# Kernel tuning notes

Hardware: AMD Instinct MI355X
Metric: run time of the kernel (lower is better)

The kernel has to match this reference:

```python
import jax, jax.numpy as jnp
import numpy as np

N, E, DN, DE, H, L = 2048, 32768, 512, 512, 8, 2
BN_EPS = 1e-5  # torch BatchNorm1d eps; eval mode with running_mean=0, running_var=1


def setup_inputs():
    key = jax.random.key(0)
    ks = jax.random.split(key, 12)
    rng = np.random.default_rng(0)
    # unique directed edges: 3E/4 upper-triangular pairs + reverses of the first E/4
    iu, ju = np.triu_indices(N, k=1)
    sel = rng.choice(iu.size, size=3 * E // 4, replace=False)
    s, d = iu[sel], ju[sel]
    src = np.concatenate([s, d[: E // 4]])
    dst = np.concatenate([d, s[: E // 4]])
    edge_index = jnp.asarray(np.stack([src, dst]).astype(np.int32))

    def p(k, shape, fan_in):
        return jax.random.normal(k, shape, jnp.float32) / np.sqrt(fan_in).astype(np.float32)

    return dict(
        x=jax.random.normal(ks[0], (N, DN), jnp.float32),
        edge_feature=jax.random.normal(ks[1], (E, DE), jnp.float32),
        node_pos=jax.random.uniform(ks[2], (N, 3), jnp.float32) * 10.0,
        inw=p(ks[3], (L, 3 * DN, DN), DN),          # MHA in_proj_weight per layer
        inb=jnp.zeros((L, 3 * DN), jnp.float32),
        ow=p(ks[4], (L, DN, DN), DN),               # MHA out_proj
        ob=jnp.zeros((L, DN), jnp.float32),
        etw=p(ks[5], (L, DE, DE), DE),              # edge_transform Linear
        etb=jnp.zeros((L, DE), jnp.float32),
        etg=jnp.ones((L, DE), jnp.float32),         # edge_transform BN gamma
        etbb=jnp.zeros((L, DE), jnp.float32),       # edge_transform BN beta
        unw=p(ks[6], (L, DN, DN + DE), DN + DE),    # update_node Linear
        unb=jnp.zeros((L, DN), jnp.float32),
        uew=p(ks[7], (L, DE, 2 * DN + 2 * DE), 2 * DN + 2 * DE),  # update_edge Linear
        ueb=jnp.zeros((L, DE), jnp.float32),
        edge_index=edge_index,
    )


def _forward(x, edge_feature, node_pos, inw, inb, ow, ob, etw, etb, etg, etbb, unw, unb, uew, ueb, edge_index):
    src, dst = edge_index[0], edge_index[1]
    n, e = x.shape[0], src.shape[0]
    hd = DN // H
    # vectorized reverse-edge lookup (mirrors the torch edge_dict)
    keys = src * n + dst
    rkeys = dst * n + src
    order = jnp.argsort(keys)
    sk = keys[order]
    pos = jnp.clip(jnp.searchsorted(sk, rkeys), 0, e - 1)
    found = sk[pos] == rkeys
    rev_idx = order[pos]
    # distance-based attention mask: -inf everywhere, 1/(dist+eps) on (symmetric) edges, 1.0 on diagonal
    diff = node_pos[src] - node_pos[dst]
    w = 1.0 / (jnp.sqrt(jnp.sum(diff * diff, axis=-1)) + 1e-6)
    mask = jnp.full((n, n), -jnp.inf, x.dtype)
    mask = mask.at[src, dst].set(w).at[dst, src].set(w)
    diag = jnp.arange(n)
    mask = mask.at[diag, diag].set(1.0)
    bn_scale = np.float32(1.0 / np.sqrt(1.0 + BN_EPS))
    nf, ef = x, edge_feature
    for l in range(L):
        rev = jnp.where(found[:, None], ef[rev_idx], 0.0)
        # MHSA over all nodes as one sequence (batch=1), eval mode (dropout off)
        qkv = nf @ inw[l].T + inb[l]
        q, k, v = [t.reshape(n, H, hd) for t in jnp.split(qkv, 3, axis=-1)]
        scores = jnp.einsum('nhd,mhd->hnm', q * np.float32(1.0 / np.sqrt(hd)), k) + mask
        attn = jax.nn.softmax(scores, axis=-1)
        ctx = jnp.einsum('hnm,mhd->nhd', attn, v).reshape(n, DN)
        x_upd = ctx @ ow[l].T + ob[l]
        # message: update_edge on [x_i, e, e_rev, x_j] (flow=target_to_source -> x_i = x[src])
        upd_edge = jnp.concatenate([nf[src], ef, rev, nf[dst]], axis=1) @ uew[l].T + ueb[l]
        # edge_transform = Linear + BN(eval) + ReLU
        te = jax.nn.relu((ef @ etw[l].T + etb[l]) * bn_scale * etg[l] + etbb[l])
        # scatter-max to subject/object nodes (empty segments -> 0, torch_scatter convention)
        subj = jax.ops.segment_max(te, src, num_segments=n)
        obj = jax.ops.segment_max(te, dst, num_segments=n)
        subj = jnp.where(jnp.isneginf(subj), 0.0, subj)
        obj = jnp.where(jnp.isneginf(obj), 0.0, obj)
        nf = jnp.concatenate([x_upd, subj + obj], axis=1) @ unw[l].T + unb[l]
        ef = upd_edge
        if l < L - 1 or L == 1:
            nf = jax.nn.relu(nf)
            ef = jax.nn.relu(ef)
    return nf, ef


def reference(x, edge_feature, node_pos, inw, inb, ow, ob, etw, etb, etg, etbb, unw, unb, uew, ueb, edge_index):
    return _forward(x, edge_feature, node_pos, inw, inb, ow, ob, etw, etb, etg, etbb, unw, unb, uew, ueb, edge_index)
```

## Files before the change

### kernel.cpp

```cpp
#include <hip/hip_runtime.h>
#include <hip/hip_bf16.h>

#define NN 2048
#define EE 32768
#define DND 512
#define NH 8
#define HD 64
#define MAXD 128
#define NEGF (-1e30f)
#define BN_SCALE 0.9999950000374997f

typedef __attribute__((ext_vector_type(8))) short bf16x8;
typedef __attribute__((ext_vector_type(4))) float f32x4;
typedef unsigned short u16;
typedef unsigned int u32;

static __device__ __forceinline__ float4 ld4(const float* p) {
    return *reinterpret_cast<const float4*>(p);
}
static __device__ __forceinline__ u16 f2b(float f) {
    __hip_bfloat16 h = __float2bfloat16(f);
    return *reinterpret_cast<u16*>(&h);
}
static __device__ __forceinline__ float b2f(u32 bits) {
    return __uint_as_float(bits << 16);
}
static __device__ __forceinline__ void gl_lds(const u16* g, u16* l) {
    __builtin_amdgcn_global_load_lds((const __attribute__((address_space(1))) void*)g,
                                     (__attribute__((address_space(3))) void*)l, 16, 0, 0);
}


__global__ __launch_bounds__(256) void init_table_k(int* __restrict__ t) {
    int i = blockIdx.x * 256 + threadIdx.x;
    t[i] = -1;
}

__global__ __launch_bounds__(256) void fill_table_k(const int* __restrict__ ei, int* __restrict__ t) {
    int e = blockIdx.x * 256 + threadIdx.x;
    if (e < EE) t[(size_t)ei[e] * NN + ei[EE + e]] = e;
}

__global__ __launch_bounds__(256) void build_rev_k(const int* __restrict__ ei, const int* __restrict__ t,
                                                   int* __restrict__ rev) {
    int e = blockIdx.x * 256 + threadIdx.x;
    if (e < EE) rev[e] = t[(size_t)ei[EE + e] * NN + ei[e]];
}

__global__ __launch_bounds__(256) void init_csr_k(int* __restrict__ adj, float* __restrict__ wadj,
                                                  int* __restrict__ cnt) {
    int i = blockIdx.x * 256 + threadIdx.x;
    if (i < NN) { cnt[i] = 1; adj[i * MAXD] = i; wadj[i * MAXD] = 1.0f; }
}

__global__ __launch_bounds__(256) void fill_csr_k(const int* __restrict__ ei, const int* __restrict__ rev,
                                                  const float* __restrict__ pos,
                                                  int* __restrict__ adj, float* __restrict__ wadj,
                                                  int* __restrict__ cnt) {
    int e = blockIdx.x * 256 + threadIdx.x;
    if (e >= EE) return;
    int s = ei[e], d = ei[EE + e];
    float dx = pos[s * 3 + 0] - pos[d * 3 + 0];
    float dy = pos[s * 3 + 1] - pos[d * 3 + 1];
    float dz = pos[s * 3 + 2] - pos[d * 3 + 2];
    float w = 1.0f / (sqrtf(dx * dx + dy * dy + dz * dz) + 1e-6f);
    int slot = atomicAdd(&cnt[s], 1);
    if (slot < MAXD) { adj[s * MAXD + slot] = d; wadj[s * MAXD + slot] = w; }
    if (rev[e] < 0) {
        slot = atomicAdd(&cnt[d], 1);
        if (slot < MAXD) { adj[d * MAXD + slot] = s; wadj[d * MAXD + slot] = w; }
    }
}

__global__ __launch_bounds__(256) void init_ecsr_k(int* __restrict__ ocnt, int* __restrict__ icnt) {
    int i = blockIdx.x * 256 + threadIdx.x;
    if (i < NN) { ocnt[i] = 0; icnt[i] = 0; }
}

__global__ __launch_bounds__(256) void fill_ecsr_k(const int* __restrict__ ei,
                                                   int* __restrict__ oadj, int* __restrict__ ocnt,
                                                   int* __restrict__ iadj, int* __restrict__ icnt) {
    int e = blockIdx.x * 256 + threadIdx.x;
    if (e >= EE) return;
    int s = ei[e], d = ei[EE + e];
    int slot = atomicAdd(&ocnt[s], 1);
    if (slot < MAXD) oadj[s * MAXD + slot] = e;
    slot = atomicAdd(&icnt[d], 1);
    if (slot < MAXD) iadj[d * MAXD + slot] = e;
}

__global__ __launch_bounds__(256) void conv_k(const float* __restrict__ src, u16* __restrict__ dst) {
    int i = (blockIdx.x * 256 + threadIdx.x) * 8;
    float4 a = ld4(src + i), b = ld4(src + i + 4);
    u16 o[8];
    o[0] = f2b(a.x); o[1] = f2b(a.y); o[2] = f2b(a.z); o[3] = f2b(a.w);
    o[4] = f2b(b.x); o[5] = f2b(b.y); o[6] = f2b(b.z); o[7] = f2b(b.w);
    *reinterpret_cast<int4*>(dst + i) = *reinterpret_cast<const int4*>(o);
}

__global__ __launch_bounds__(256) void gather_max_k(const u16* __restrict__ te,
                                                    const int* __restrict__ oadj, const int* __restrict__ ocnt,
                                                    const int* __restrict__ iadj, const int* __restrict__ icnt,
                                                    u16* __restrict__ sums)
{
    const int i = blockIdx.x;
    const int c2 = threadIdx.x;
    float ms0 = 0.f, ms1 = 0.f, mo0 = 0.f, mo1 = 0.f;
    int no = ocnt[i]; if (no > MAXD) no = MAXD;
    for (int s = 0; s < no; ++s) {
        const int e = oadj[i * MAXD + s];
        const u32 v = *reinterpret_cast<const u32*>(te + (size_t)e * DND + c2 * 2);
        ms0 = fmaxf(ms0, b2f(v & 0xffffu));
        ms1 = fmaxf(ms1, b2f(v >> 16));
    }
    int ni = icnt[i]; if (ni > MAXD) ni = MAXD;
    for (int s = 0; s < ni; ++s) {
        const int e = iadj[i * MAXD + s];
        const u32 v = *reinterpret_cast<const u32*>(te + (size_t)e * DND + c2 * 2);
        mo0 = fmaxf(mo0, b2f(v & 0xffffu));
        mo1 = fmaxf(mo1, b2f(v >> 16));
    }
    const u32 r = (u32)f2b(ms0 + mo0) | ((u32)f2b(ms1 + mo1) << 16);
    *reinterpret_cast<u32*>(sums + (size_t)i * DND + c2 * 2) = r;
}

template <int MODE, int EPI, int WF32, int WBF16, int GY>
__global__ __launch_bounds__(256) void mgemm_k(
    const u16* __restrict__ WS, u32 a_off, u32 b_off, const float* __restrict__ bias,
    float* __restrict__ Cf, u16* __restrict__ Cb, int M, int Nc, int K,
    u32 g0_off, u32 g1_off, u32 gz_off,
    const int* __restrict__ srcv, const int* __restrict__ dstv, const int* __restrict__ revv,
    const float* __restrict__ eg, const float* __restrict__ eb)
{
    __shared__ u16 As2[2][8192];
    __shared__ u16 Bs2[2][8192];
    const int tid = threadIdx.x, lane = tid & 63, w = tid >> 6;
    const int wr = w >> 1, wc = w & 1;
    const int b = blockIdx.x;
    const int xcd = b & 7, kb = b >> 3;
    const int bm = ((kb / GY) * 8 + xcd) * 128;
    const int bn = (kb % GY) * 128;

    const int rl = lane >> 3;
    const u32 lx = (u32)(((lane & 7) ^ rl) * 8);

    u32 offA0[4], offA1[4], offB[4];
#pragma unroll
    for (int q = 0; q < 4; ++q) {
        const int ra = bm + w * 32 + q * 8 + rl;
        if (MODE == 0) {
            offA0[q] = a_off + (u32)ra * (u32)K + lx;
        } else {
            offA0[q] = g0_off + (u32)ra * 512u + lx;
            offA1[q] = g1_off + (u32)ra * 512u + lx;
        }
        offB[q] = b_off + (u32)(bn + w * 32 + q * 8 + rl) * (u32)K + lx;
    }

    const int nks = K >> 6;
    const int kq = lane >> 4, li = lane & 15;

    auto stage = [&](int t, int buf) {
        const u32 k0 = (u32)t * 64u;
        const int seg = (MODE == 0) ? 0 : (int)(k0 >> 9);
#pragma unroll
        for (int q = 0; q < 4; ++q) {
            u32 oa = (MODE == 0) ? offA0[q] : (seg == 0 ? offA0[q] : offA1[q]);
            const u32 koff = (MODE == 0) ? k0 : (k0 & 511u);
            gl_lds(WS + oa + koff, &As2[buf][(w * 32 + q * 8) * 64]);
        }
#pragma unroll
        for (int q = 0; q < 4; ++q)
            gl_lds(WS + offB[q] + k0, &Bs2[buf][(w * 32 + q * 8) * 64]);
    };

    f32x4 acc[4][4] = {};
    const int baseA = (wr * 64 + li) * 64 + ((kq ^ (li & 7)) * 8);
    const int baseB = (wc * 64 + li) * 64 + ((kq ^ (li & 7)) * 8);

    stage(0, 0);
    for (int t = 0; t < nks; ++t) {
        const int cur = t & 1;
        if (t + 1 < nks) stage(t + 1, cur ^ 1);
        if (t + 1 < nks) asm volatile("s_waitcnt vmcnt(8)" ::: "memory");
        else             asm volatile("s_waitcnt vmcnt(0)" ::: "memory");
        __builtin_amdgcn_s_barrier();
        __builtin_amdgcn_sched_barrier(0);
#pragma unroll
        for (int sub = 0; sub < 2; ++sub) {
            const int sx = sub << 5;
            bf16x8 af[4], bf[4];
#pragma unroll
            for (int m = 0; m < 4; ++m)
                af[m] = *reinterpret_cast<const bf16x8*>(&As2[cur][(baseA + m * 1024) ^ sx]);
#pragma unroll
            for (int n = 0; n < 4; ++n)
                bf[n] = *reinterpret_cast<const bf16x8*>(&Bs2[cur][(baseB + n * 1024) ^ sx]);
#pragma unroll
            for (int m = 0; m < 4; ++m)
#pragma unroll
                for (int n = 0; n < 4; ++n)
                    acc[m][n] = __builtin_amdgcn_mfma_f32_16x16x32_bf16(af[m], bf[n], acc[m][n], 0, 0, 0);
        }
        __builtin_amdgcn_s_barrier();
        __builtin_amdgcn_sched_barrier(0);
    }

    float bsv[4], scv[4], shv[4];
#pragma unroll
    for (int n = 0; n < 4; ++n) {
        const int col = bn + wc * 64 + n * 16 + li;
        bsv[n] = bias[col];
        if (EPI == 2) { scv[n] = BN_SCALE * eg[col]; shv[n] = eb[col]; }
    }
#pragma unroll
    for (int m = 0; m < 4; ++m) {
#pragma unroll
        for (int n = 0; n < 4; ++n) {
            const int col = bn + wc * 64 + n * 16 + li;
#pragma unroll
            for (int i = 0; i < 4; ++i) {
                float v = acc[m][n][i] + bsv[n];
                if (EPI == 2) v = fmaxf(fmaf(v, scv[n], shv[n]), 0.f);
                else if (EPI == 1) v = fmaxf(v, 0.f);
                const int r = bm + wr * 64 + m * 16 + (lane >> 4) * 4 + i;
                if (WF32) Cf[(size_t)r * Nc + col] = v;
                if (WBF16) Cb[(size_t)r * Nc + col] = f2b(v);
            }
        }
    }
}

template <int MODE, int EPI, int WF32, int WBF16>
__global__ __launch_bounds__(512, 2) void mgemm256_k(
    const u16* __restrict__ WS, u32 a_off, u32 b_off, const float* __restrict__ bias,
    float* __restrict__ Cf, u16* __restrict__ Cb, int M, int Nc, int K,
    u32 g0_off, u32 g1_off, u32 gz_off,
    const int* __restrict__ srcv, const int* __restrict__ dstv, const int* __restrict__ revv,
    const float* __restrict__ eg, const float* __restrict__ eb)
{
    __shared__ u16 SB[65536];
    const int tid = threadIdx.x, lane = tid & 63, w = tid >> 6;
    const int wr = w >> 2, wc = w & 3;
    const int b = blockIdx.x;
    const int bm = ((b & 7) + 8 * (b >> 4)) * 256;
    const int bn = ((b >> 3) & 1) * 256;

    const int rl = lane >> 3;
    const u32 lx = (u32)(((lane & 7) ^ rl) * 8);

    u32 offA0[4], offA1[4], offA2[4], offA3[4], offB[4];
#pragma unroll
    for (int q = 0; q < 4; ++q) {
        const int ra = bm + w * 32 + q * 8 + rl;
        if (MODE == 0) {
            offA0[q] = a_off + (u32)ra * (u32)K + lx;
        } else {
            offA0[q] = g0_off + (u32)srcv[ra] * 512u + lx;
            offA1[q] = g1_off + (u32)ra * 512u + lx;
            const int rv = revv[ra];
            offA2[q] = (rv >= 0 ? g1_off + (u32)rv * 512u : gz_off) + lx;
            offA3[q] = g0_off + (u32)dstv[ra] * 512u + lx;
        }
        offB[q] = b_off + (u32)(bn + w * 32 + q * 8 + rl) * (u32)K + lx;
    }

    const int nks = K >> 6;
    const int kq = lane >> 4, li = lane & 15;

    auto stageA2 = [&](int t, int buf, int q0) {
        const u32 k0 = (u32)t * 64u;
        const int seg = (MODE == 0) ? 0 : (int)(k0 >> 9);
        const u32 koff = (MODE == 0) ? k0 : (k0 & 511u);
#pragma unroll
        for (int q = q0; q < q0 + 2; ++q) {
            u32 oa;
            if (MODE == 0) oa = offA0[q];
            else           oa = (seg == 0 ? offA0[q] : seg == 1 ? offA1[q] : seg == 2 ? offA2[q] : offA3[q]);
            gl_lds(WS + oa + koff, &SB[buf * 16384 + (w * 32 + q * 8) * 64]);
        }
    };
    auto stageB2 = [&](int t, int buf, int q0) {
        const u32 k0 = (u32)t * 64u;
#pragma unroll
        for (int q = q0; q < q0 + 2; ++q)
            gl_lds(WS + offB[q] + k0, &SB[32768 + buf * 16384 + (w * 32 + q * 8) * 64]);
    };

    f32x4 acc[8][4] = {};
    const int baseA = (wr * 128 + li) * 64 + ((kq ^ (li & 7)) * 8);
    const int baseB = (wc * 64 + li) * 64 + ((kq ^ (li & 7)) * 8);

    stageA2(0, 0, 0); stageA2(0, 0, 2); stageB2(0, 0, 0); stageB2(0, 0, 2);
    for (int t = 0; t < nks; ++t) {
        const int cur = t & 1;
        const bool pf = (t + 1 < nks);
        if (pf) {
            stageA2(t + 1, cur ^ 1, 0);
            asm volatile("s_waitcnt vmcnt(2)" ::: "memory");
        } else {
            asm volatile("s_waitcnt vmcnt(0)" ::: "memory");
        }
        __builtin_amdgcn_s_barrier();
        __builtin_amdgcn_sched_barrier(0);
#pragma unroll
        for (int sub = 0; sub < 2; ++sub) {
            const int sx = sub << 5;
            bf16x8 bf[4];
#pragma unroll
            for (int n = 0; n < 4; ++n)
                bf[n] = *reinterpret_cast<const bf16x8*>(&SB[(32768 + cur * 16384 + baseB + n * 1024) ^ sx]);
#pragma unroll
            for (int mh = 0; mh < 2; ++mh) {
                if (pf) {
                    if (sub == 0 && mh == 0)      stageA2(t + 1, cur ^ 1, 2);
                    else if (sub == 0 && mh == 1) stageB2(t + 1, cur ^ 1, 0);
                    else if (sub == 1 && mh == 0) stageB2(t + 1, cur ^ 1, 2);
                }
                bf16x8 af[4];
#pragma unroll
                for (int m = 0; m < 4; ++m)
                    af[m] = *reinterpret_cast<const bf16x8*>(&SB[(cur * 16384 + baseA + (mh * 4 + m) * 1024) ^ sx]);
                __builtin_amdgcn_sched_barrier(0);
                __builtin_amdgcn_s_setprio(1);
#pragma unroll
                for (int m = 0; m < 4; ++m)
#pragma unroll
                    for (int n = 0; n < 4; ++n)
                        acc[mh * 4 + m][n] =
                            __builtin_amdgcn_mfma_f32_16x16x32_bf16(af[m], bf[n], acc[mh * 4 + m][n], 0, 0, 0);
                __builtin_amdgcn_s_setprio(0);
                __builtin_amdgcn_sched_barrier(0);
            }
        }
        __builtin_amdgcn_s_barrier();
        __builtin_amdgcn_sched_barrier(0);
    }

    float bsv[4], scv[4], shv[4];
#pragma unroll
    for (int n = 0; n < 4; ++n) {
        const int col = bn + wc * 64 + n * 16 + li;
        bsv[n] = bias[col];
        if (EPI == 2) { scv[n] = BN_SCALE * eg[col]; shv[n] = eb[col]; }
    }
#pragma unroll
    for (int m = 0; m < 8; ++m) {
#pragma unroll
        for (int n = 0; n < 4; ++n) {
            const int col = bn + wc * 64 + n * 16 + li;
#pragma unroll
            for (int i = 0; i < 4; ++i) {
                float v = acc[m][n][i] + bsv[n];
                if (EPI == 2) v = fmaxf(fmaf(v, scv[n], shv[n]), 0.f);
                else if (EPI == 1) v = fmaxf(v, 0.f);
                const int r = bm + wr * 128 + m * 16 + (lane >> 4) * 4 + i;
                if (WF32) Cf[(size_t)r * Nc + col] = v;
                if (WBF16) Cb[(size_t)r * Nc + col] = f2b(v);
            }
        }
    }
}

__global__ __launch_bounds__(256) void attn_sp_k(const float* __restrict__ qkv,
                                                 const int* __restrict__ adj,
                                                 const float* __restrict__ wadj,
                                                 const int* __restrict__ cnt,
                                                 u16* __restrict__ ctxb)
{
    const int i = blockIdx.x;
    const int wv = threadIdx.x >> 6, lane = threadIdx.x & 63;
    const int h = blockIdx.y * 4 + wv;
    __shared__ float qs[4][64];
    qs[wv][lane] = qkv[(size_t)i * 1536 + h * HD + lane] * 0.125f;
    __syncthreads();
    int deg = cnt[i];
    if (deg > MAXD) deg = MAXD;
    float m = -3.0e38f, lsum = 0.f, c = 0.f;
    for (int base = 0; base < deg; base += 64) {
        int nn_ = deg - base; if (nn_ > 64) nn_ = 64;
        int j = 0;
        float s = NEGF;
        if (lane < nn_) {
            j = adj[i * MAXD + base + lane];
            const float wgt = wadj[i * MAXD + base + lane];
            const float* kr = qkv + (size_t)j * 1536 + DND + h * HD;
            float accd = 0.f;
#pragma unroll
            for (int d4 = 0; d4 < 16; ++d4) {
                float4 kv = ld4(kr + d4 * 4);
                accd = fmaf(qs[wv][d4 * 4 + 0], kv.x, accd);
                accd = fmaf(qs[wv][d4 * 4 + 1], kv.y, accd);
                accd = fmaf(qs[wv][d4 * 4 + 2], kv.z, accd);
                accd = fmaf(qs[wv][d4 * 4 + 3], kv.w, accd);
            }
            s = accd + wgt;
        }
        float mloc = s;
#pragma unroll
        for (int o = 1; o < 64; o <<= 1) mloc = fmaxf(mloc, __shfl_xor(mloc, o, 64));
        const float mnew = fmaxf(m, mloc);
        const float alpha = __expf(m - mnew);
        const float p = (lane < nn_) ? __expf(s - mnew) : 0.f;
        float ps = p;
#pragma unroll
        for (int o = 1; o < 64; o <<= 1) ps += __shfl_xor(ps, o, 64);
        lsum = lsum * alpha + ps;
        c *= alpha;
        for (int l = 0; l < nn_; ++l) {
            const float pj = __shfl(p, l, 64);
            const int jj = __shfl(j, l, 64);
            c = fmaf(pj, qkv[(size_t)jj * 1536 + 2 * DND + h * HD + lane], c);
        }
        m = mnew;
    }
    ctxb[(size_t)i * DND + h * HD + lane] = f2b(c / lsum);
}

extern "C" void kernel_launch(void* const* d_in, const int* in_sizes, int n_in,
                              void* d_out, int out_size, void* d_ws, size_t ws_size,
                              hipStream_t stream)
{
    const float* x    = (const float*)d_in[0];
    const float* efin = (const float*)d_in[1];
    const float* pos  = (const float*)d_in[2];
    const float* inw  = (const float*)d_in[3];
    const float* inb  = (const float*)d_in[4];
    const float* ow   = (const float*)d_in[5];
    const float* ob   = (const float*)d_in[6];
    const float* etw  = (const float*)d_in[7];
    const float* etb  = (const float*)d_in[8];
    const float* etg  = (const float*)d_in[9];
    const float* etbb = (const float*)d_in[10];
    const float* unw  = (const float*)d_in[11];
    const float* unb  = (const float*)d_in[12];
    const float* uew  = (const float*)d_in[13];
    const float* ueb  = (const float*)d_in[14];
    const int*   ei   = (const int*)d_in[15];

    float* W = (float*)d_ws;
    float* qkv   = W;
    u16*   te    = (u16*)W;
    int*   rev   = (int*)(W + 8388608);
    u16*   zero  = (u16*)(W + 8421376);
    int*   adj   = (int*)(W + 8421888);
    float* wadj  = W + 8684032;
    int*   cnt   = (int*)(W + 8946176);
    int*   oadj  = (int*)(W + 8948224);
    int*   ocnt  = (int*)(W + 9210368);
    int*   iadj  = (int*)(W + 9212416);
    int*   icnt  = (int*)(W + 9474560);
    u16*   ctxb  = (u16*)(W + 9476608);
    u16*   xupdb = (u16*)(W + 10000896);
    u16*   sums  = (u16*)(W + 10525184);
    u16*   nfb   = (u16*)(W + 11049472);
    u16*   wbf   = (u16*)(W + 11573760);
    u16*   efbA  = (u16*)(W + 14457344);
    u16*   efbB  = (u16*)(W + 22845952);
    int*   table = (int*)efbA;

    u16* inwb = wbf;
    u16* owb  = wbf + 1572864;
    u16* etwb = wbf + 2097152;
    u16* unwb = wbf + 2621440;
    u16* uewb = wbf + 3670016;

    float* out_nf = (float*)d_out;
    float* out_ef = out_nf + (size_t)NN * DND;

    const int* srcv = ei;
    const int* dstv = ei + EE;

    const u16* WSu = (const u16*)d_ws;
    auto uoff = [&](const void* p) { return (u32)((const u16*)p - WSu); };

    init_table_k<<<NN * NN / 256, 256, 0, stream>>>(table);
    fill_table_k<<<EE / 256, 256, 0, stream>>>(ei, table);
    build_rev_k<<<EE / 256, 256, 0, stream>>>(ei, table, rev);
    init_csr_k<<<NN / 256, 256, 0, stream>>>(adj, wadj, cnt);
    fill_csr_k<<<EE / 256, 256, 0, stream>>>(ei, rev, pos, adj, wadj, cnt);
    init_ecsr_k<<<NN / 256, 256, 0, stream>>>(ocnt, icnt);
    fill_ecsr_k<<<EE / 256, 256, 0, stream>>>(ei, oadj, ocnt, iadj, icnt);
    hipMemsetAsync(zero, 0, 2048, stream);

    conv_k<<<1572864 / 2048, 256, 0, stream>>>(inw, inwb);
    conv_k<<<524288 / 2048, 256, 0, stream>>>(ow, owb);
    conv_k<<<524288 / 2048, 256, 0, stream>>>(etw, etwb);
    conv_k<<<1048576 / 2048, 256, 0, stream>>>(unw, unwb);
    conv_k<<<2097152 / 2048, 256, 0, stream>>>(uew, uewb);
    conv_k<<<1048576 / 2048, 256, 0, stream>>>(x, nfb);
    conv_k<<<16777216 / 2048, 256, 0, stream>>>(efin, efbA);

    for (int l = 0; l < 2; ++l) {
        const u16* efb_cur = l ? efbB : efbA;
        const u16* inwb_l = inwb + (size_t)l * 786432;
        const u16* owb_l  = owb  + (size_t)l * 262144;
        const u16* etwb_l = etwb + (size_t)l * 262144;
        const u16* unwb_l = unwb + (size_t)l * 524288;
        const u16* uewb_l = uewb + (size_t)l * 1048576;
        const float* inb_l  = inb  + (size_t)l * 1536;
        const float* ob_l   = ob   + (size_t)l * 512;
        const float* etb_l  = etb  + (size_t)l * 512;
        const float* etg_l  = etg  + (size_t)l * 512;
        const float* etbb_l = etbb + (size_t)l * 512;
        const float* unb_l  = unb  + (size_t)l * 512;
        const float* ueb_l  = ueb  + (size_t)l * 512;

        mgemm_k<0, 0, 1, 0, 12><<<192, 256, 0, stream>>>(
            WSu, uoff(nfb), uoff(inwb_l), inb_l, qkv, nullptr, NN, 1536, DND,
            0, 0, 0, nullptr, nullptr, nullptr, nullptr, nullptr);

        attn_sp_k<<<dim3(NN, 2), 256, 0, stream>>>(qkv, adj, wadj, cnt, ctxb);

        mgemm_k<0, 0, 0, 1, 4><<<64, 256, 0, stream>>>(
            WSu, uoff(ctxb), uoff(owb_l), ob_l, nullptr, xupdb, NN, DND, DND,
            0, 0, 0, nullptr, nullptr, nullptr, nullptr, nullptr);

        mgemm256_k<0, 2, 0, 1><<<256, 512, 0, stream>>>(
            WSu, uoff(efb_cur), uoff(etwb_l), etb_l, nullptr, te, EE, DND, DND,
            0, 0, 0, nullptr, nullptr, nullptr, etg_l, etbb_l);

        gather_max_k<<<NN, 256, 0, stream>>>(te, oadj, ocnt, iadj, icnt, sums);

        if (l == 0)
            mgemm256_k<1, 1, 0, 1><<<256, 512, 0, stream>>>(
                WSu, 0, uoff(uewb_l), ueb_l, nullptr, efbB, EE, DND, 2048,
                uoff(nfb), uoff(efb_cur), uoff(zero), srcv, dstv, rev, nullptr, nullptr);
        else
            mgemm256_k<1, 0, 1, 0><<<256, 512, 0, stream>>>(
                WSu, 0, uoff(uewb_l), ueb_l, out_ef, nullptr, EE, DND, 2048,
                uoff(nfb), uoff(efb_cur), uoff(zero), srcv, dstv, rev, nullptr, nullptr);

        if (l == 0)
            mgemm_k<2, 1, 0, 1, 4><<<64, 256, 0, stream>>>(
                WSu, 0, uoff(unwb_l), unb_l, nullptr, nfb, NN, DND, 1024,
                uoff(xupdb), uoff(sums), 0, nullptr, nullptr, nullptr, nullptr, nullptr);
        else
            mgemm_k<2, 0, 1, 0, 4><<<64, 256, 0, stream>>>(
                WSu, 0, uoff(unwb_l), unb_l, out_nf, nullptr, NN, DND, 1024,
                uoff(xupdb), uoff(sums), 0, nullptr, nullptr, nullptr, nullptr, nullptr);
    }
}
```

Before: 463.8 us.

## Fuse setup kernels into fewer launches and store QKV in bf16

New measurement: 431.2 us. 7.0% less time.

```diff
diff --git a/kernel.cpp b/kernel.cpp
--- a/kernel.cpp
+++ b/kernel.cpp
@@ -31,67 +31,74 @@
 }
 
 
-__global__ __launch_bounds__(256) void init_table_k(int* __restrict__ t) {
+__global__ __launch_bounds__(256) void setup_init_k(int* __restrict__ t,
+                                                    int* __restrict__ adj, float* __restrict__ wadj,
+                                                    int* __restrict__ cnt,
+                                                    int* __restrict__ ocnt, int* __restrict__ icnt,
+                                                    u16* __restrict__ zero)
+{
     int i = blockIdx.x * 256 + threadIdx.x;
     t[i] = -1;
-}
-
-__global__ __launch_bounds__(256) void fill_table_k(const int* __restrict__ ei, int* __restrict__ t) {
-    int e = blockIdx.x * 256 + threadIdx.x;
-    if (e < EE) t[(size_t)ei[e] * NN + ei[EE + e]] = e;
-}
-
-__global__ __launch_bounds__(256) void build_rev_k(const int* __restrict__ ei, const int* __restrict__ t,
-                                                   int* __restrict__ rev) {
-    int e = blockIdx.x * 256 + threadIdx.x;
-    if (e < EE) rev[e] = t[(size_t)ei[EE + e] * NN + ei[e]];
-}
-
-__global__ __launch_bounds__(256) void init_csr_k(int* __restrict__ adj, float* __restrict__ wadj,
-                                                  int* __restrict__ cnt) {
-    int i = blockIdx.x * 256 + threadIdx.x;
-    if (i < NN) { cnt[i] = 1; adj[i * MAXD] = i; wadj[i * MAXD] = 1.0f; }
-}
-
-__global__ __launch_bounds__(256) void fill_csr_k(const int* __restrict__ ei, const int* __restrict__ rev,
-                                                  const float* __restrict__ pos,
-                                                  int* __restrict__ adj, float* __restrict__ wadj,
-                                                  int* __restrict__ cnt) {
+    if (i < NN) {
+        cnt[i] = 1; adj[i * MAXD] = i; wadj[i * MAXD] = 1.0f;
+        ocnt[i] = 0; icnt[i] = 0;
+    }
+    if (i < 1024) zero[i] = 0;
+}
+
+__global__ __launch_bounds__(256) void fill_scatter_k(const int* __restrict__ ei, int* __restrict__ t,
+                                                      int* __restrict__ oadj, int* __restrict__ ocnt,
+                                                      int* __restrict__ iadj, int* __restrict__ icnt)
+{
     int e = blockIdx.x * 256 + threadIdx.x;
     if (e >= EE) return;
     int s = ei[e], d = ei[EE + e];
+    t[(size_t)s * NN + d] = e;
+    int slot = atomicAdd(&ocnt[s], 1);
+    if (slot < MAXD) oadj[s * MAXD + slot] = e;
+    slot = atomicAdd(&icnt[d], 1);
+    if (slot < MAXD) iadj[d * MAXD + slot] = e;
+}
+
+__global__ __launch_bounds__(256) void rev_csr_k(const int* __restrict__ ei, const int* __restrict__ t,
+                                                 const float* __restrict__ pos,
+                                                 int* __restrict__ rev,
+                                                 int* __restrict__ adj, float* __restrict__ wadj,
+                                                 int* __restrict__ cnt)
+{
+    int e = blockIdx.x * 256 + threadIdx.x;
+    if (e >= EE) return;
+    int s = ei[e], d = ei[EE + e];
+    int r = t[(size_t)d * NN + s];
+    rev[e] = r;
     float dx = pos[s * 3 + 0] - pos[d * 3 + 0];
     float dy = pos[s * 3 + 1] - pos[d * 3 + 1];
     float dz = pos[s * 3 + 2] - pos[d * 3 + 2];
     float w = 1.0f / (sqrtf(dx * dx + dy * dy + dz * dz) + 1e-6f);
     int slot = atomicAdd(&cnt[s], 1);
     if (slot < MAXD) { adj[s * MAXD + slot] = d; wadj[s * MAXD + slot] = w; }
-    if (rev[e] < 0) {
+    if (r < 0) {
         slot = atomicAdd(&cnt[d], 1);
         if (slot < MAXD) { adj[d * MAXD + slot] = s; wadj[d * MAXD + slot] = w; }
     }
 }
 
-__global__ __launch_bounds__(256) void init_ecsr_k(int* __restrict__ ocnt, int* __restrict__ icnt) {
-    int i = blockIdx.x * 256 + threadIdx.x;
-    if (i < NN) { ocnt[i] = 0; icnt[i] = 0; }
-}
-
-__global__ __launch_bounds__(256) void fill_ecsr_k(const int* __restrict__ ei,
-                                                   int* __restrict__ oadj, int* __restrict__ ocnt,
-                                                   int* __restrict__ iadj, int* __restrict__ icnt) {
-    int e = blockIdx.x * 256 + threadIdx.x;
-    if (e >= EE) return;
-    int s = ei[e], d = ei[EE + e];
-    int slot = atomicAdd(&ocnt[s], 1);
-    if (slot < MAXD) oadj[s * MAXD + slot] = e;
-    slot = atomicAdd(&icnt[d], 1);
-    if (slot < MAXD) iadj[d * MAXD + slot] = e;
-}
-
-__global__ __launch_bounds__(256) void conv_k(const float* __restrict__ src, u16* __restrict__ dst) {
-    int i = (blockIdx.x * 256 + threadIdx.x) * 8;
-    float4 a = ld4(src + i), b = ld4(src + i + 4);
+__global__ __launch_bounds__(256) void conv_all_k(
+    const float* __restrict__ x, const float* __restrict__ inw, const float* __restrict__ ow,
+    const float* __restrict__ etw, const float* __restrict__ unw, const float* __restrict__ uew,
+    const float* __restrict__ efin, u16* __restrict__ dst)
+{
+    size_t i = ((size_t)blockIdx.x * 256 + threadIdx.x) * 8;
+    const float* s;
+    size_t off;
+    if (i < 1048576)      { s = x;    off = i; }
+    else if (i < 2621440) { s = inw;  off = i - 1048576; }
+    else if (i < 3145728) { s = ow;   off = i - 2621440; }
+    else if (i < 3670016) { s = etw;  off = i - 3145728; }
+    else if (i < 4718592) { s = unw;  off = i - 3670016; }
+    else if (i < 6815744) { s = uew;  off = i - 4718592; }
+    else                  { s = efin; off = i - 6815744; }
+    float4 a = ld4(s + off), b = ld4(s + off + 4);
     u16 o[8];
     o[0] = f2b(a.x); o[1] = f2b(a.y); o[2] = f2b(a.z); o[3] = f2b(a.w);
     o[4] = f2b(b.x); o[5] = f2b(b.y); o[6] = f2b(b.z); o[7] = f2b(b.w);
@@ -362,7 +369,7 @@
     }
 }
 
-__global__ __launch_bounds__(256) void attn_sp_k(const float* __restrict__ qkv,
+__global__ __launch_bounds__(256) void attn_sp_k(const u16* __restrict__ qkvb,
                                                  const int* __restrict__ adj,
                                                  const float* __restrict__ wadj,
                                                  const int* __restrict__ cnt,
@@ -372,7 +379,7 @@
     const int wv = threadIdx.x >> 6, lane = threadIdx.x & 63;
     const int h = blockIdx.y * 4 + wv;
     __shared__ float qs[4][64];
-    qs[wv][lane] = qkv[(size_t)i * 1536 + h * HD + lane] * 0.125f;
+    qs[wv][lane] = b2f((u32)qkvb[(size_t)i * 1536 + h * HD + lane]) * 0.125f;
     __syncthreads();
     int deg = cnt[i];
     if (deg > MAXD) deg = MAXD;
@@ -384,15 +391,29 @@
         if (lane < nn_) {
             j = adj[i * MAXD + base + lane];
             const float wgt = wadj[i * MAXD + base + lane];
-            const float* kr = qkv + (size_t)j * 1536 + DND + h * HD;
+            const u16* kr = qkvb + (size_t)j * 1536 + DND + h * HD;
             float accd = 0.f;
 #pragma unroll
-            for (int d4 = 0; d4 < 16; ++d4) {
-                float4 kv = ld4(kr + d4 * 4);
-                accd = fmaf(qs[wv][d4 * 4 + 0], kv.x, accd);
-                accd = fmaf(qs[wv][d4 * 4 + 1], kv.y, accd);
-                accd = fmaf(qs[wv][d4 * 4 + 2], kv.z, accd);
-                accd = fmaf(qs[wv][d4 * 4 + 3], kv.w, accd);
+            for (int cq = 0; cq < 4; ++cq) {
+                uint4 kv = *reinterpret_cast<const uint4*>(kr + cq * 16);
+                const float* qp = &qs[wv][cq * 16];
+                accd = fmaf(qp[0],  b2f(kv.x & 0xffffu), accd);
+                accd = fmaf(qp[1],  b2f(kv.x >> 16), accd);
+                accd = fmaf(qp[2],  b2f(kv.y & 0xffffu), accd);
+                accd = fmaf(qp[3],  b2f(kv.y >> 16), accd);
+                accd = fmaf(qp[4],  b2f(kv.z & 0xffffu), accd);
+                accd = fmaf(qp[5],  b2f(kv.z >> 16), accd);
+                accd = fmaf(qp[6],  b2f(kv.w & 0xffffu), accd);
+                accd = fmaf(qp[7],  b2f(kv.w >> 16), accd);
+                uint4 kv2 = *reinterpret_cast<const uint4*>(kr + cq * 16 + 8);
+                accd = fmaf(qp[8],  b2f(kv2.x & 0xffffu), accd);
+                accd = fmaf(qp[9],  b2f(kv2.x >> 16), accd);
+                accd = fmaf(qp[10], b2f(kv2.y & 0xffffu), accd);
+                accd = fmaf(qp[11], b2f(kv2.y >> 16), accd);
+                accd = fmaf(qp[12], b2f(kv2.z & 0xffffu), accd);
+                accd = fmaf(qp[13], b2f(kv2.z >> 16), accd);
+                accd = fmaf(qp[14], b2f(kv2.w & 0xffffu), accd);
+                accd = fmaf(qp[15], b2f(kv2.w >> 16), accd);
             }
             s = accd + wgt;
         }
@@ -410,7 +431,7 @@
         for (int l = 0; l < nn_; ++l) {
             const float pj = __shfl(p, l, 64);
             const int jj = __shfl(j, l, 64);
-            c = fmaf(pj, qkv[(size_t)jj * 1536 + 2 * DND + h * HD + lane], c);
+            c = fmaf(pj, b2f((u32)qkvb[(size_t)jj * 1536 + 2 * DND + h * HD + lane]), c);
         }
         m = mnew;
     }
@@ -439,7 +460,7 @@
     const int*   ei   = (const int*)d_in[15];
 
     float* W = (float*)d_ws;
-    float* qkv   = W;
+    u16*   qkvb  = (u16*)W;
     u16*   te    = (u16*)W;
     int*   rev   = (int*)(W + 8388608);
     u16*   zero  = (u16*)(W + 8421376);
@@ -474,22 +495,10 @@
     const u16* WSu = (const u16*)d_ws;
     auto uoff = [&](const void* p) { return (u32)((const u16*)p - WSu); };
 
-    init_table_k<<<NN * NN / 256, 256, 0, stream>>>(table);
-    fill_table_k<<<EE / 256, 256, 0, stream>>>(ei, table);
-    build_rev_k<<<EE / 256, 256, 0, stream>>>(ei, table, rev);
-    init_csr_k<<<NN / 256, 256, 0, stream>>>(adj, wadj, cnt);
-    fill_csr_k<<<EE / 256, 256, 0, stream>>>(ei, rev, pos, adj, wadj, cnt);
-    init_ecsr_k<<<NN / 256, 256, 0, stream>>>(ocnt, icnt);
-    fill_ecsr_k<<<EE / 256, 256, 0, stream>>>(ei, oadj, ocnt, iadj, icnt);
-    hipMemsetAsync(zero, 0, 2048, stream);
-
-    conv_k<<<1572864 / 2048, 256, 0, stream>>>(inw, inwb);
-    conv_k<<<524288 / 2048, 256, 0, stream>>>(ow, owb);
-    conv_k<<<524288 / 2048, 256, 0, stream>>>(etw, etwb);
-    conv_k<<<1048576 / 2048, 256, 0, stream>>>(unw, unwb);
-    conv_k<<<2097152 / 2048, 256, 0, stream>>>(uew, uewb);
-    conv_k<<<1048576 / 2048, 256, 0, stream>>>(x, nfb);
-    conv_k<<<16777216 / 2048, 256, 0, stream>>>(efin, efbA);
+    setup_init_k<<<NN * NN / 256, 256, 0, stream>>>(table, adj, wadj, cnt, ocnt, icnt, zero);
+    fill_scatter_k<<<EE / 256, 256, 0, stream>>>(ei, table, oadj, ocnt, iadj, icnt);
+    rev_csr_k<<<EE / 256, 256, 0, stream>>>(ei, table, pos, rev, adj, wadj, cnt);
+    conv_all_k<<<11520, 256, 0, stream>>>(x, inw, ow, etw, unw, uew, efin, nfb);
 
     for (int l = 0; l < 2; ++l) {
         const u16* efb_cur = l ? efbB : efbA;
@@ -506,11 +515,11 @@
         const float* unb_l  = unb  + (size_t)l * 512;
         const float* ueb_l  = ueb  + (size_t)l * 512;
 
-        mgemm_k<0, 0, 1, 0, 12><<<192, 256, 0, stream>>>(
-            WSu, uoff(nfb), uoff(inwb_l), inb_l, qkv, nullptr, NN, 1536, DND,
+        mgemm_k<0, 0, 0, 1, 12><<<192, 256, 0, stream>>>(
+            WSu, uoff(nfb), uoff(inwb_l), inb_l, nullptr, qkvb, NN, 1536, DND,
             0, 0, 0, nullptr, nullptr, nullptr, nullptr, nullptr);
 
-        attn_sp_k<<<dim3(NN, 2), 256, 0, stream>>>(qkv, adj, wadj, cnt, ctxb);
+        attn_sp_k<<<dim3(NN, 2), 256, 0, stream>>>(qkvb, adj, wadj, cnt, ctxb);
 
         mgemm_k<0, 0, 0, 1, 4><<<64, 256, 0, stream>>>(
             WSu, uoff(ctxb), uoff(owb_l), ob_l, nullptr, xupdb, NN, DND, DND,
```
